# Kernel optimization log

Measured on AMD Instinct MI355X. Metric: run time of the kernel, lower is better.

Reference implementation:

```python
import math
import jax, jax.numpy as jnp
import numpy as np

D_MODEL = 1024
NUM_SCALES = 4
STATE_SIZE = 16
EXPAND = 2
D_INNER = D_MODEL * EXPAND
D_PER_SCALE = D_INNER // NUM_SCALES
BATCH, SEQ = 4, 4096


def _make_A_log():
    base = np.arange(1, STATE_SIZE + 1, dtype=np.float32)  # (N,)
    parts = [np.broadcast_to(base * (2.0 ** i), (D_PER_SCALE, STATE_SIZE)) for i in range(NUM_SCALES)]
    A = np.concatenate(parts, axis=0)  # (d_inner, N)
    return jnp.asarray(np.log(A))


def setup_inputs() -> dict:
    key = jax.random.key(0)
    ks = jax.random.split(key, 8)
    scale = 0.02
    x = jax.random.normal(ks[0], (BATCH, SEQ, D_MODEL), dtype=jnp.float32)
    W_in = jax.random.normal(ks[1], (2 * D_INNER, D_MODEL), dtype=jnp.float32) * scale
    W_B = jax.random.normal(ks[2], (STATE_SIZE, D_INNER), dtype=jnp.float32) * scale
    W_C = jax.random.normal(ks[3], (STATE_SIZE, D_INNER), dtype=jnp.float32) * scale
    W_dt = jax.random.normal(ks[4], (D_INNER, D_INNER), dtype=jnp.float32) * scale
    # dt bias: log of dt_init ~ Uniform in log-space between 1e-3 and 1e-1
    u = jax.random.uniform(ks[5], (D_INNER,), dtype=jnp.float32)
    b_dt = u * (math.log(0.1) - math.log(0.001)) + math.log(0.001)
    W_out = jax.random.normal(ks[6], (D_MODEL, D_INNER), dtype=jnp.float32) * scale
    A_log = _make_A_log()
    D = jnp.ones((D_INNER,), dtype=jnp.float32)
    output_gate = jnp.zeros((1,), dtype=jnp.float32)
    return {"x": x, "W_in": W_in, "A_log": A_log, "W_B": W_B, "W_C": W_C,
            "W_dt": W_dt, "b_dt": b_dt, "D": D, "output_gate": output_gate, "W_out": W_out}


def _selective_scan(x_ssm, A, B_mat, C_mat, dt):
    # x_ssm: (B,L,d), A: (d,N), B_mat/C_mat: (B,L,N), dt: (B,L,d)
    b, L, d = x_ssm.shape
    N = A.shape[1]
    h0 = jnp.zeros((b, d, N), dtype=jnp.float32)

    def step(h, inp):
        dt_t, B_t, C_t, x_t = inp  # (B,d),(B,N),(B,N),(B,d)
        A_bar = jnp.exp(jnp.minimum(dt_t[..., None] * A, 20.0))       # (B,d,N)
        B_bar = dt_t[..., None] * B_t[:, None, :]                      # (B,d,N)
        h = A_bar * h + B_bar * x_t[..., None]
        y_t = jnp.einsum('bdn,bn->bd', h, C_t)
        return h, y_t

    xs = (jnp.swapaxes(dt, 0, 1), jnp.swapaxes(B_mat, 0, 1),
          jnp.swapaxes(C_mat, 0, 1), jnp.swapaxes(x_ssm, 0, 1))
    _, ys = jax.lax.scan(step, h0, xs)   # ys: (L,B,d)
    return jnp.swapaxes(ys, 0, 1)


def reference(x, W_in, A_log, W_B, W_C, W_dt, b_dt, D, output_gate, W_out):
    xz = jnp.einsum('bld,ed->ble', x, W_in)          # (B,L,2*d_inner)
    x_ssm, z = jnp.split(xz, 2, axis=-1)
    A = -jnp.exp(A_log.astype(jnp.float32))           # (d_inner,N)
    B_mat = jnp.einsum('bld,nd->bln', x_ssm, W_B)
    C_mat = jnp.einsum('bld,nd->bln', x_ssm, W_C)
    dt = jax.nn.softplus(jnp.einsum('bld,ed->ble', x_ssm, W_dt) + b_dt)
    y = _selective_scan(x_ssm.astype(jnp.float32), A,
                        B_mat.astype(jnp.float32), C_mat.astype(jnp.float32),
                        dt.astype(jnp.float32))
    y = y + x_ssm * D[None, None, :]
    y = y * jax.nn.silu(z)
    out = jnp.einsum('ble,de->bld', y, W_out) * jax.nn.sigmoid(output_gate)
    return out
```

## Files before the change

kernel.cpp:

```cpp
#include <hip/hip_runtime.h>
#include <hip/hip_bf16.h>
#include <math.h>

#define D_MODEL 1024
#define D_INNER 2048
#define NSTATE  16
#define BATCH   4
#define SEQ     4096
#define MTOT    (BATCH*SEQ)
#define SDT     2176
#define NCATP   2304
#define NBIG    6272
#define NCHUNK  16
#define CLEN    (SEQ/NCHUNK)
#define N1      (2*D_INNER)

typedef __attribute__((ext_vector_type(8))) __bf16 bf16x8;
typedef __attribute__((ext_vector_type(4))) float f32x4;

__device__ __forceinline__ float b2f(unsigned short u){
  return __uint_as_float(((unsigned int)u) << 16);
}
__device__ __forceinline__ unsigned short f2b(float f){
  unsigned int u = __float_as_uint(f);
  u = (u + 0x7FFFu + ((u >> 16) & 1u)) >> 16;
  return (unsigned short)u;
}
__device__ __forceinline__ float softplus_f(float x){
  float r = log1pf(__expf(-fabsf(x)));
  return x > 0.f ? x + r : r;
}

__device__ __forceinline__ void async16(unsigned short* lds, const unsigned short* g){
  __builtin_amdgcn_global_load_lds(
      (const __attribute__((address_space(1))) unsigned int*)g,
      (__attribute__((address_space(3))) unsigned int*)lds, 16, 0, 0);
}

__global__ void cvt_f2b_kernel(const float* __restrict__ src,
                               unsigned short* __restrict__ dst){
  int i = (blockIdx.x * 256 + threadIdx.x) * 4;
  float4 v = *(const float4*)(src + i);
  *(ushort2*)(dst + i)     = (ushort2){f2b(v.x), f2b(v.y)};
  *(ushort2*)(dst + i + 2) = (ushort2){f2b(v.z), f2b(v.w)};
}

__global__ void concat_w_kernel(const float* __restrict__ Wdt,
                                const float* __restrict__ WB,
                                const float* __restrict__ WC,
                                unsigned short* __restrict__ Wcat){
  int idx = blockIdx.x * 256 + threadIdx.x;
  int row = idx >> 9;
  int q   = idx & 511;
  float4 v;
  if      (row < 2048) v = *(const float4*)(Wdt + ((size_t)row * 2048 + q * 4));
  else if (row < 2064) v = *(const float4*)(WB  + ((size_t)(row - 2048) * 2048 + q * 4));
  else if (row < 2080) v = *(const float4*)(WC  + ((size_t)(row - 2064) * 2048 + q * 4));
  else                 v = make_float4(0.f, 0.f, 0.f, 0.f);
  unsigned short* p = Wcat + (size_t)idx * 4;
  *(ushort2*)(p)     = (ushort2){f2b(v.x), f2b(v.y)};
  *(ushort2*)(p + 2) = (ushort2){f2b(v.z), f2b(v.w)};
}

__global__ __launch_bounds__(256) void transpose_cvt_kernel(
    const float* __restrict__ Win, unsigned short* __restrict__ WxT){
  __shared__ float t[64][65];
  const int e0 = blockIdx.x * 64;
  const int k0 = blockIdx.y * 64;
  const int r  = threadIdx.x >> 2;
  const int q  = threadIdx.x & 3;
  #pragma unroll
  for (int jj = 0; jj < 4; jj++){
    float4 v = *(const float4*)&Win[(size_t)(e0 + r) * 1024 + k0 + q*16 + jj*4];
    t[r][q*16 + jj*4 + 0] = v.x; t[r][q*16 + jj*4 + 1] = v.y;
    t[r][q*16 + jj*4 + 2] = v.z; t[r][q*16 + jj*4 + 3] = v.w;
  }
  __syncthreads();
  #pragma unroll
  for (int jj = 0; jj < 2; jj++){
    ushort4 o;
    o.x = f2b(t[q*16 + jj*8 + 0][r]); o.y = f2b(t[q*16 + jj*8 + 1][r]);
    o.z = f2b(t[q*16 + jj*8 + 2][r]); o.w = f2b(t[q*16 + jj*8 + 3][r]);
    *(ushort4*)&WxT[(size_t)(k0 + r) * 2048 + e0 + q*16 + jj*8] = o;
    o.x = f2b(t[q*16 + jj*8 + 4][r]); o.y = f2b(t[q*16 + jj*8 + 5][r]);
    o.z = f2b(t[q*16 + jj*8 + 6][r]); o.w = f2b(t[q*16 + jj*8 + 7][r]);
    *(ushort4*)&WxT[(size_t)(k0 + r) * 2048 + e0 + q*16 + jj*8 + 4] = o;
  }
}

__global__ void zfill_kernel(unsigned short* __restrict__ p){
  p[blockIdx.x * 256 + threadIdx.x] = 0;
}

template<int MODE, int K, int GX, int GY>
__global__ __launch_bounds__(512, 1) void gemm_bt(
    const unsigned short* __restrict__ A,
    const unsigned short* __restrict__ W,
    unsigned short* __restrict__ o0,
    unsigned short* __restrict__ o1,
    unsigned short* __restrict__ o2,
    float* __restrict__ of,
    const float* __restrict__ bias)
{
  const int tid  = threadIdx.x;
  const int lane = tid & 63;
  const int w    = tid >> 6;
  const int wm   = w >> 1;
  const int wn   = w & 1;
  const int m16  = lane & 15, q = lane >> 4;

  constexpr int NWG = GX * GY;
  int flat = blockIdx.y * GX + blockIdx.x;
  flat = (flat & 7) * (NWG >> 3) + (flat >> 3);
  const int bm = flat / GX;
  const int bn = flat - bm * GX;

  __shared__ unsigned short sA[2][16384];
  __shared__ unsigned short sB[2][8192];

  f32x4 acc[4][4];
  #pragma unroll
  for (int i = 0; i < 4; i++)
    #pragma unroll
    for (int j = 0; j < 4; j++) acc[i][j] = (f32x4){0.f, 0.f, 0.f, 0.f};

  const int ch = (tid & 7) ^ ((tid >> 3) & 7);
  const unsigned short* Ag = A + (size_t)(bm * 256 + (tid >> 3)) * K + ch * 8;
  const unsigned short* Wg = W + (size_t)(bn * 128 + (tid >> 3)) * K + ch * 8;

#define STAGE_A(buf, h, t) do { \
    async16(&sA[buf][(h)*8192 + w*512],        Ag + (size_t)((h)*128    )*K + (t)*64); \
    async16(&sA[buf][(h)*8192 + 4096 + w*512], Ag + (size_t)((h)*128 + 64)*K + (t)*64); \
  } while(0)
#define STAGE_B(buf, t) do { \
    async16(&sB[buf][w*512],        Wg + (size_t)(t)*64); \
    async16(&sB[buf][4096 + w*512], Wg + (size_t)64*K + (t)*64); \
  } while(0)

#define LDA(dst, buf) do { \
    _Pragma("unroll") for (int mt = 0; mt < 4; mt++) \
    _Pragma("unroll") for (int kk = 0; kk < 2; kk++) { \
      const int row_ = wm*64 + mt*16 + m16; \
      dst[mt][kk] = *(const bf16x8*)&sA[buf][row_*64 + (((kk*4 + q) ^ (m16 & 7)) << 3)]; \
    } } while(0)
#define LDB(dst, buf, nh) do { \
    _Pragma("unroll") for (int nt = 0; nt < 2; nt++) \
    _Pragma("unroll") for (int kk = 0; kk < 2; kk++) { \
      const int row_ = wn*64 + (nh)*32 + nt*16 + m16; \
      dst[nt][kk] = *(const bf16x8*)&sB[buf][row_*64 + (((kk*4 + q) ^ (m16 & 7)) << 3)]; \
    } } while(0)

#define MMAQ(Aa, Bb, NH) do { \
    __builtin_amdgcn_s_setprio(1); \
    _Pragma("unroll") for (int kk = 0; kk < 2; kk++) \
    _Pragma("unroll") for (int mt = 0; mt < 4; mt++) \
    _Pragma("unroll") for (int nt = 0; nt < 2; nt++) \
      acc[mt][(NH)*2 + nt] = __builtin_amdgcn_mfma_f32_16x16x32_bf16( \
          Aa[mt][kk], Bb[nt][kk], acc[mt][(NH)*2 + nt], 0, 0, 0); \
    __builtin_amdgcn_s_setprio(0); \
  } while(0)

#define BAR()  asm volatile("s_barrier" ::: "memory")
#define LGK0() asm volatile("s_waitcnt lgkmcnt(0)" ::: "memory")

  STAGE_A(0, 0, 0); STAGE_A(0, 1, 0); STAGE_B(0, 0);
  STAGE_A(1, 0, 1); STAGE_A(1, 1, 1);
  asm volatile("s_waitcnt vmcnt(4)" ::: "memory");
  BAR();

  auto run_iter = [&](int t0, bool last) {
    bf16x8 a[4][2], b[2][2];
    LDA(a, 0); LDB(b, 0, 0);
    STAGE_B(1, t0 + 1);
    BAR(); LGK0();
    MMAQ(a, b, 0);
    BAR();
    LDB(b, 0, 1);
    if (!last) { STAGE_A(0, 0, t0 + 2); STAGE_A(0, 1, t0 + 2); }
    BAR(); LGK0();
    MMAQ(a, b, 1);
    if (last) asm volatile("s_waitcnt vmcnt(0)" ::: "memory");
    else      asm volatile("s_waitcnt vmcnt(4)" ::: "memory");
    BAR();
    LDA(a, 1); LDB(b, 1, 0);
    if (!last) STAGE_B(0, t0 + 2);
    BAR(); LGK0();
    MMAQ(a, b, 0);
    BAR();
    LDB(b, 1, 1);
    if (!last) { STAGE_A(1, 0, t0 + 3); STAGE_A(1, 1, t0 + 3); }
    BAR(); LGK0();
    MMAQ(a, b, 1);
    if (!last) asm volatile("s_waitcnt vmcnt(4)" ::: "memory");
    BAR();
  };

  constexpr int NIT = K >> 7;
  #pragma unroll 1
  for (int j = 0; j < NIT - 1; j++) run_iter(2 * j, false);
  run_iter(2 * (NIT - 1), true);

  float gscale = 1.f;
  if (MODE == 2) gscale = 1.f / (1.f + __expf(-bias[0]));

  const int r0 = bm * 256 + wm * 64 + (q << 2);
  const int c0 = bn * 128 + wn * 64 + m16;
  #pragma unroll
  for (int mt = 0; mt < 4; mt++) {
    #pragma unroll
    for (int nt = 0; nt < 4; nt++) {
      const int col = c0 + nt * 16;
      #pragma unroll
      for (int i = 0; i < 4; i++) {
        const int row = r0 + mt * 16 + i;
        float v = acc[mt][nt][i];
        if (MODE == 0) {
          if      (col < 2048) o0[(size_t)row * D_INNER + col] = f2b(v);
          else if (col < 4096) o1[(size_t)row * D_INNER + (col - 2048)] = f2b(v);
          else if (col < 6144) o2[(size_t)row * SDT + (col - 4096)] =
                                   f2b(softplus_f(v + bias[col - 4096]));
          else if (col < 6176) o2[(size_t)row * SDT + 2048 + (col - 6144)] = f2b(v);
        } else if (MODE == 2) {
          of[(size_t)row * D_MODEL + col] = v * gscale;
        } else {
          if (row < 2080) o0[(size_t)row * D_MODEL + col] = f2b(v);
        }
      }
    }
  }
#undef STAGE_A
#undef STAGE_B
#undef LDA
#undef LDB
#undef MMAQ
#undef BAR
#undef LGK0
}

__global__ __launch_bounds__(256) void scan_passA(
    const unsigned short* __restrict__ dtBC,
    const unsigned short* __restrict__ xs,
    const float* __restrict__ Alog,
    float* __restrict__ Pb, float* __restrict__ Sb)
{
  const int d = blockIdx.x * 256 + threadIdx.x;
  const int b = blockIdx.y;
  const int c = blockIdx.z;

  float a[NSTATE];
  #pragma unroll
  for (int n = 0; n < NSTATE; n++) a[n] = -__expf(Alog[d * NSTATE + n]);

  float P[NSTATE], S[NSTATE];
  #pragma unroll
  for (int n = 0; n < NSTATE; n++) { P[n] = 1.f; S[n] = 0.f; }

  __shared__ float sB[16][16];
  const size_t bL = (size_t)b * SEQ;
  const int t0c = c * CLEN;
  const int lt = threadIdx.x >> 4, ln = threadIdx.x & 15;

  for (int t0 = t0c; t0 < t0c + CLEN; t0 += 16) {
    __syncthreads();
    sB[lt][ln] = b2f(dtBC[(bL + t0 + lt) * SDT + 2048 + ln]);
    __syncthreads();
    for (int tt = 0; tt < 16; tt++) {
      const size_t rw = bL + t0 + tt;
      const float dt = b2f(dtBC[rw * SDT + d]);
      const float x  = b2f(xs[rw * D_INNER + d]);
      const float dtx = dt * x;
      #pragma unroll
      for (int n = 0; n < NSTATE; n++) {
        const float ab = __expf(dt * a[n]);
        P[n] *= ab;
        S[n] = ab * S[n] + dtx * sB[tt][n];
      }
    }
  }
  const size_t base = (((size_t)c * BATCH + b) * D_INNER + d) * NSTATE;
  #pragma unroll
  for (int n = 0; n < NSTATE; n += 4) {
    *(f32x4*)&Pb[base + n] = (f32x4){P[n], P[n+1], P[n+2], P[n+3]};
    *(f32x4*)&Sb[base + n] = (f32x4){S[n], S[n+1], S[n+2], S[n+3]};
  }
}

__global__ __launch_bounds__(256) void scan_passB(float* __restrict__ Pb,
                                                  const float* __restrict__ Sb)
{
  const size_t j = (size_t)blockIdx.x * 256 + threadIdx.x;
  const size_t stride = (size_t)BATCH * D_INNER * NSTATE;
  float h = 0.f;
  for (int c = 0; c < NCHUNK; c++) {
    const size_t idx = (size_t)c * stride + j;
    const float p = Pb[idx];
    const float s = Sb[idx];
    Pb[idx] = h;
    h = p * h + s;
  }
}

__global__ __launch_bounds__(256) void scan_passC(
    const unsigned short* __restrict__ dtBC,
    const unsigned short* __restrict__ xs,
    const unsigned short* __restrict__ zb,
    const float* __restrict__ Alog,
    const float* __restrict__ Dv,
    const float* __restrict__ Hb,
    unsigned short* __restrict__ yb)
{
  const int d = blockIdx.x * 256 + threadIdx.x;
  const int b = blockIdx.y;
  const int c = blockIdx.z;

  float a[NSTATE];
  #pragma unroll
  for (int n = 0; n < NSTATE; n++) a[n] = -__expf(Alog[d * NSTATE + n]);

  float h[NSTATE];
  const size_t base = (((size_t)c * BATCH + b) * D_INNER + d) * NSTATE;
  #pragma unroll
  for (int n = 0; n < NSTATE; n += 4) {
    f32x4 v = *(const f32x4*)&Hb[base + n];
    h[n] = v.x; h[n+1] = v.y; h[n+2] = v.z; h[n+3] = v.w;
  }
  const float Dd = Dv[d];

  __shared__ float sB[16][16];
  __shared__ float sC[16][16];
  const size_t bL = (size_t)b * SEQ;
  const int t0c = c * CLEN;
  const int lt = threadIdx.x >> 4, ln = threadIdx.x & 15;

  for (int t0 = t0c; t0 < t0c + CLEN; t0 += 16) {
    __syncthreads();
    {
      const size_t rwb = (bL + t0 + lt) * SDT + 2048;
      sB[lt][ln] = b2f(dtBC[rwb + ln]);
      sC[lt][ln] = b2f(dtBC[rwb + 16 + ln]);
    }
    __syncthreads();
    for (int tt = 0; tt < 16; tt++) {
      const size_t rw = bL + t0 + tt;
      const float dt = b2f(dtBC[rw * SDT + d]);
      const float x  = b2f(xs[rw * D_INNER + d]);
      const float z  = b2f(zb[rw * D_INNER + d]);
      const float dtx = dt * x;
      float y = 0.f;
      #pragma unroll
      for (int n = 0; n < NSTATE; n++) {
        const float ab = __expf(dt * a[n]);
        h[n] = ab * h[n] + dtx * sB[tt][n];
        y += h[n] * sC[tt][n];
      }
      y = (y + x * Dd) * (z / (1.f + __expf(-z)));
      yb[rw * D_INNER + d] = f2b(y);
    }
  }
}

extern "C" void kernel_launch(void* const* d_in, const int* in_sizes, int n_in,
                              void* d_out, int out_size, void* d_ws, size_t ws_size,
                              hipStream_t stream)
{
  const float* x    = (const float*)d_in[0];
  const float* Win  = (const float*)d_in[1];
  const float* Alog = (const float*)d_in[2];
  const float* WB   = (const float*)d_in[3];
  const float* WC   = (const float*)d_in[4];
  const float* Wdt  = (const float*)d_in[5];
  const float* bdt  = (const float*)d_in[6];
  const float* Dv   = (const float*)d_in[7];
  const float* gate = (const float*)d_in[8];
  const float* Wout = (const float*)d_in[9];
  float* outp = (float*)d_out;

  char* ws = (char*)d_ws;
  unsigned short* xs    = (unsigned short*)(ws + 0);
  unsigned short* zy    = (unsigned short*)(ws + 67108864);
  unsigned short* dtBC  = (unsigned short*)(ws + 134217728);
  unsigned short* WxT   = (unsigned short*)(ws + 205520896);
  unsigned short* Woutb = (unsigned short*)(ws + 213909504);

  char* ob = (char*)d_out;
  float* Pb = (float*)(ob + 0);
  float* Sb = (float*)(ob + 8388608);
  unsigned short* Acomp = (unsigned short*)(ob + 0);
  unsigned short* Wcomb = (unsigned short*)(ob + 16777216);
  unsigned short* xb    = (unsigned short*)(ob + 33554432);

  cvt_f2b_kernel<<<16384, 256, 0, stream>>>(x, xb);
  cvt_f2b_kernel<<<4096, 256, 0, stream>>>(Win, Wcomb);
  cvt_f2b_kernel<<<2048, 256, 0, stream>>>(Wout, Woutb);
  concat_w_kernel<<<(NCATP * D_INNER / 4) / 256, 256, 0, stream>>>(Wdt, WB, WC, Acomp);
  transpose_cvt_kernel<<<dim3(32, 16), 256, 0, stream>>>(Win, WxT);
  zfill_kernel<<<384, 256, 0, stream>>>(Wcomb + (size_t)6176 * 1024);

  gemm_bt<3, 2048, 8, 9><<<dim3(8, 9), 512, 0, stream>>>(
      Acomp, WxT, Wcomb + (size_t)4096 * 1024, nullptr, nullptr, nullptr, nullptr);

  gemm_bt<0, D_MODEL, NBIG / 128, MTOT / 256><<<dim3(NBIG / 128, MTOT / 256), 512, 0, stream>>>(
      xb, Wcomb, xs, zy, dtBC, nullptr, bdt);

  scan_passA<<<dim3(D_INNER / 256, BATCH, NCHUNK), 256, 0, stream>>>(
      dtBC, xs, Alog, Pb, Sb);
  scan_passB<<<(BATCH * D_INNER * NSTATE) / 256, 256, 0, stream>>>(Pb, Sb);
  scan_passC<<<dim3(D_INNER / 256, BATCH, NCHUNK), 256, 0, stream>>>(
      dtBC, xs, zy, Alog, Dv, Pb, zy);
  gemm_bt<2, D_INNER, D_MODEL / 128, MTOT / 256><<<dim3(D_MODEL / 128, MTOT / 256), 512, 0, stream>>>(
      zy, Woutb, nullptr, nullptr, nullptr, outp, gate);
}
```

Measured before the change: 1.177 ms.

## Triple-buffer GEMM shared-memory staging to prefetch two K-tiles ahead

Replaces the double-buffered, manually unrolled two-tile K loop in the bf16 MFMA GEMM with a three-stage ring buffer in shared memory. Loads are issued two tiles ahead, and the wait allows six outstanding loads. The aim is to hide more global-load latency behind the MFMA work. In exchange, shared-memory use grows by half, which may limit blocks per CU, and buffer indices are now computed at runtime.

```diff
diff --git a/kernel.cpp b/kernel.cpp
--- a/kernel.cpp
+++ b/kernel.cpp
@@ -115,8 +115,8 @@
   const int bm = flat / GX;
   const int bn = flat - bm * GX;
 
-  __shared__ unsigned short sA[2][16384];
-  __shared__ unsigned short sB[2][8192];
+  __shared__ unsigned short sA[3][16384];
+  __shared__ unsigned short sB[3][8192];
 
   f32x4 acc[4][4];
   #pragma unroll
@@ -164,41 +164,31 @@
 #define LGK0() asm volatile("s_waitcnt lgkmcnt(0)" ::: "memory")
 
   STAGE_A(0, 0, 0); STAGE_A(0, 1, 0); STAGE_B(0, 0);
-  STAGE_A(1, 0, 1); STAGE_A(1, 1, 1);
-  asm volatile("s_waitcnt vmcnt(4)" ::: "memory");
+  STAGE_A(1, 0, 1); STAGE_A(1, 1, 1); STAGE_B(1, 1);
+  asm volatile("s_waitcnt vmcnt(6)" ::: "memory");
   BAR();
 
-  auto run_iter = [&](int t0, bool last) {
+  constexpr int NT = K >> 6;
+  int cr = 0, cs = 2;
+  #pragma unroll 1
+  for (int t = 0; t < NT; t++) {
     bf16x8 a[4][2], b[2][2];
-    LDA(a, 0); LDB(b, 0, 0);
-    STAGE_B(1, t0 + 1);
+    const bool st = (t + 2 < NT);
+    LDA(a, cr); LDB(b, cr, 0);
+    if (st) { STAGE_A(cs, 0, t + 2); STAGE_A(cs, 1, t + 2); }
     BAR(); LGK0();
     MMAQ(a, b, 0);
     BAR();
-    LDB(b, 0, 1);
-    if (!last) { STAGE_A(0, 0, t0 + 2); STAGE_A(0, 1, t0 + 2); }
+    LDB(b, cr, 1);
+    if (st) STAGE_B(cs, t + 2);
     BAR(); LGK0();
     MMAQ(a, b, 1);
-    if (last) asm volatile("s_waitcnt vmcnt(0)" ::: "memory");
-    else      asm volatile("s_waitcnt vmcnt(4)" ::: "memory");
+    if (st)                 asm volatile("s_waitcnt vmcnt(6)" ::: "memory");
+    else if (t + 1 < NT)    asm volatile("s_waitcnt vmcnt(0)" ::: "memory");
     BAR();
-    LDA(a, 1); LDB(b, 1, 0);
-    if (!last) STAGE_B(0, t0 + 2);
-    BAR(); LGK0();
-    MMAQ(a, b, 0);
-    BAR();
-    LDB(b, 1, 1);
-    if (!last) { STAGE_A(1, 0, t0 + 3); STAGE_A(1, 1, t0 + 3); }
-    BAR(); LGK0();
-    MMAQ(a, b, 1);
-    if (!last) asm volatile("s_waitcnt vmcnt(4)" ::: "memory");
-    BAR();
-  };
-
-  constexpr int NIT = K >> 7;
-  #pragma unroll 1
-  for (int j = 0; j < NIT - 1; j++) run_iter(2 * j, false);
-  run_iter(2 * (NIT - 1), true);
+    cr = (cr == 2) ? 0 : cr + 1;
+    cs = (cs == 2) ? 0 : cs + 1;
+  }
 
   float gscale = 1.f;
   if (MODE == 2) gscale = 1.f / (1.f + __expf(-bias[0]));
```

Measured after the change: 1.096 ms. 6.9% less time.
